# Kernel tuning notes

Hardware: AMD Instinct MI355X
Metric: run time of the kernel (lower is better)

Reference implementation:

```python
import jax, jax.numpy as jnp
import numpy as np

N_NODES = 50000
N_EDGES = 800000
F_IN = 32
F_OUT = 32
NB = 4  # basis terms per dimension


def linear_basis(x, n):
    # Piecewise-linear 'hat' basis on [-1, 1] with n equispaced centers.
    # f_k(x) = max(0, 1 - |x - c_k| / dx),  c_k = linspace(-1, 1, n), dx = 2/(n-1)
    centers = jnp.linspace(-1.0, 1.0, n, dtype=x.dtype)
    dx = 2.0 / (n - 1)
    return jnp.maximum(0.0, 1.0 - jnp.abs(x[:, None] - centers) / dx)  # [E, n]


def setup_inputs() -> dict:
    key = jax.random.key(0)
    k0, k1, k2, k3, k4 = jax.random.split(key, 5)
    x_i = jax.random.normal(k0, (N_NODES, F_IN), dtype=jnp.float32)
    x_j = jax.random.normal(k1, (N_NODES, F_IN), dtype=jnp.float32)
    edge_index = jax.random.randint(k2, (2, N_EDGES), 0, N_NODES)  # row0=target, row1=source
    edge_attr = jax.random.uniform(k3, (N_EDGES, 2), dtype=jnp.float32,
                                   minval=-1.0, maxval=1.0)
    # torch init: uniform_(-0.05, 0.05) on [NB, NB, F_IN, F_OUT]
    weight = jax.random.uniform(k4, (NB, NB, F_IN, F_OUT), dtype=jnp.float32,
                                minval=-0.05, maxval=0.05)
    return {"x_i": x_i, "x_j": x_j, "edge_index": edge_index,
            "edge_attr": edge_attr, "weight": weight}


def reference(x_i, x_j, edge_index, edge_attr, weight):
    dst = edge_index[0]  # aggregation target nodes
    src = edge_index[1]  # source nodes (features gathered from x_j)

    bx = linear_basis(edge_attr[:, 0], NB)            # [E, NB]
    by = linear_basis(edge_attr[:, 1], NB)            # [E, NB]
    b = (bx[:, :, None] * by[:, None, :]).reshape(-1, NB * NB)  # [E, NB*NB]

    feat = x_j[src]                                   # [E, F_IN] edge gather
    w = weight.reshape(NB * NB, F_IN, F_OUT)          # [K, F_IN, F_OUT]
    msg = jnp.einsum('ek,ei,kio->eo', b, feat, w)     # [E, F_OUT]

    # weighted scatter-add to target nodes
    out = jax.ops.segment_sum(msg, dst, num_segments=x_i.shape[0])  # [N, F_OUT]
    return out
```

## Files before the change

kernel.cpp:

```cpp
#include <hip/hip_runtime.h>

typedef short short8 __attribute__((ext_vector_type(8)));
typedef float f32x4 __attribute__((ext_vector_type(4)));

#define NB 4
#define F 32
#define EPB 512
#define SCHUNK 2048
#define MAXNBLK 1024


__device__ __forceinline__ int cell_of(float ax, float ay) {
    float tx = (ax + 1.0f) * 1.5f;
    float ty = (ay + 1.0f) * 1.5f;
    int kx = (int)tx; if (kx > 2) kx = 2; if (kx < 0) kx = 0;
    int ky = (int)ty; if (ky > 2) ky = 2; if (ky < 0) ky = 0;
    return kx * 3 + ky;
}

__device__ __forceinline__ short f2bf(float f) {
    unsigned u = __float_as_uint(f);
    unsigned r = (u + 0x7FFFu + ((u >> 16) & 1u)) >> 16;
    return (short)r;
}

__global__ __launch_bounds__(256) void hist_kernel(
    const float* __restrict__ attr, int E, int* __restrict__ counts)
{
    __shared__ int h[9];
    int b = blockIdx.x, t = threadIdx.x;
    if (t < 9) h[t] = 0;
    __syncthreads();
    int start = b * SCHUNK, end = min(start + SCHUNK, E);
    for (int e = start + t; e < end; e += 256) {
        float2 a = reinterpret_cast<const float2*>(attr)[e];
        atomicAdd(&h[cell_of(a.x, a.y)], 1);
    }
    __syncthreads();
    if (t < 9) counts[b * 9 + t] = h[t];
}

__global__ __launch_bounds__(512) void scan_kernel(
    int* __restrict__ ws, int* __restrict__ counts, int nblk)
{
    __shared__ int s[MAXNBLK * 9];
    __shared__ int tot[9];
    __shared__ int coff[9];
    int n = nblk * 9;
    for (int i = threadIdx.x; i < n; i += 512) s[i] = counts[i];
    __syncthreads();
    if (threadIdx.x < 9) {
        int c = threadIdx.x, run = 0;
        for (int b = 0; b < nblk; ++b) {
            int v = s[b * 9 + c];
            s[b * 9 + c] = run;
            run += v;
        }
        tot[c] = run;
    }
    __syncthreads();
    if (threadIdx.x == 0) {
        int off = 0, boff = 0;
        for (int c = 0; c < 9; ++c) {
            ws[c] = off;  coff[c] = off;
            ws[16 + c] = boff;
            off  += tot[c];
            boff += (tot[c] + EPB - 1) / EPB;
        }
        ws[9] = off;
        ws[16 + 9] = boff;
    }
    __syncthreads();
    for (int i = threadIdx.x; i < n; i += 512)
        counts[i] = s[i] + coff[i % 9];
}

__global__ __launch_bounds__(256) void scatter_kernel(
    const float* __restrict__ attr, int E,
    const int* __restrict__ bases, int* __restrict__ sorted)
{
    __shared__ int cur[9];
    int b = blockIdx.x, t = threadIdx.x;
    if (t < 9) cur[t] = bases[b * 9 + t];
    __syncthreads();
    int start = b * SCHUNK, end = min(start + SCHUNK, E);
    for (int e = start + t; e < end; e += 256) {
        float2 a = reinterpret_cast<const float2*>(attr)[e];
        int c = cell_of(a.x, a.y);
        int pos = atomicAdd(&cur[c], 1);
        sorted[pos] = e;
    }
}

__global__ __launch_bounds__(256) void bconv_mfma(
    const float* __restrict__ x_j, const int* __restrict__ ei,
    const float* __restrict__ attr, const float* __restrict__ weight,
    const int* __restrict__ ws, const int* __restrict__ sorted,
    float* __restrict__ out, int E)
{
    int b = blockIdx.x;
    const int* blkoff = ws + 16;
    if (b >= blkoff[9]) return;
    int c = 0;
    #pragma unroll
    for (int q = 1; q < 9; ++q) c += (b >= blkoff[q]) ? 1 : 0;
    int kx0 = c / 3, ky0 = c - 3 * (c / 3);
    int local  = b - blkoff[c];
    int cstart = ws[c];
    int cend   = ws[c + 1];
    int pstart = cstart + local * EPB;
    int pend   = min(pstart + EPB, cend);

    int t     = threadIdx.x;
    int wid   = t >> 6;
    int lane  = t & 63;
    int row16 = lane & 15;
    int hi    = lane >> 4;
    int edge4 = lane >> 2;
    int chunk = lane & 3;

    __shared__ short featb[4][4][4][16][8];
    __shared__ int   dstl[4][16];

    short8 wb[4][2];
    #pragma unroll
    for (int kk = 0; kk < 4; ++kk) {
        int ks = (kx0 + (kk >> 1)) * NB + (ky0 + (kk & 1));
        const float* wp = weight + (size_t)ks * F * F;
        #pragma unroll
        for (int n = 0; n < 2; ++n) {
            short8 v;
            #pragma unroll
            for (int j = 0; j < 8; ++j)
                v[j] = f2bf(wp[(8 * hi + j) * F + row16 + 16 * n]);
            wb[kk][n] = v;
        }
    }

    int wstart = pstart + wid * (EPB / 4);
    int wend   = min(wstart + (EPB / 4), pend);
    if (wstart >= wend) return;

    int   dst0; float ax0, ay0; float4 fa0, fb0; bool v0;
    auto load = [&](int tstart, int& dst, float& ax, float& ay,
                    float4& fa, float4& fb, bool& valid) {
        int p = tstart + edge4;
        valid = p < wend;
        int pp = valid ? p : wstart;
        int e  = sorted[pp];
        dst = ei[e];
        int srcn = ei[E + e];
        float2 a = reinterpret_cast<const float2*>(attr)[e];
        ax = a.x; ay = a.y;
        const float4* xr = reinterpret_cast<const float4*>(x_j + (size_t)srcn * F);
        fa = xr[chunk * 2];
        fb = xr[chunk * 2 + 1];
    };

    int ntiles = (wend - wstart + 15) >> 4;
    load(wstart, dst0, ax0, ay0, fa0, fb0, v0);

    for (int tt = 0; tt < ntiles; ++tt) {
        float fx  = (ax0 + 1.0f) * 1.5f - (float)kx0;
        float fy  = (ay0 + 1.0f) * 1.5f - (float)ky0;
        float bxa = 1.0f - fx, bya = 1.0f - fy;
        float bc[4] = { bxa * bya, bxa * fy, fx * bya, fx * fy };
        float fl[8] = { fa0.x, fa0.y, fa0.z, fa0.w, fb0.x, fb0.y, fb0.z, fb0.w };
        #pragma unroll
        for (int kk = 0; kk < 4; ++kk) {
            float s = v0 ? bc[kk] : 0.0f;
            short8 sv;
            #pragma unroll
            for (int j = 0; j < 8; ++j) sv[j] = f2bf(fl[j] * s);
            *reinterpret_cast<short8*>(&featb[wid][kk][chunk][edge4][0]) = sv;
        }
        if (chunk == 0) dstl[wid][edge4] = v0 ? dst0 : -1;

        if (tt + 1 < ntiles)
            load(wstart + (tt + 1) * 16, dst0, ax0, ay0, fa0, fb0, v0);

        f32x4 acc0 = {0.f, 0.f, 0.f, 0.f}, acc1 = {0.f, 0.f, 0.f, 0.f};
        #pragma unroll
        for (int kk = 0; kk < 4; ++kk) {
            short8 a = *reinterpret_cast<const short8*>(&featb[wid][kk][hi][row16][0]);
            acc0 = __builtin_amdgcn_mfma_f32_16x16x32_bf16(a, wb[kk][0], acc0, 0, 0, 0);
            acc1 = __builtin_amdgcn_mfma_f32_16x16x32_bf16(a, wb[kk][1], acc1, 0, 0, 0);
        }

        #pragma unroll
        for (int r = 0; r < 4; ++r) {
            int d = dstl[wid][hi * 4 + r];
            if (d >= 0) {
                atomicAdd(&out[(size_t)d * F + row16],      acc0[r]);
                atomicAdd(&out[(size_t)d * F + 16 + row16], acc1[r]);
            }
        }
    }
}

__global__ __launch_bounds__(256) void bconv_fallback(
    const float* __restrict__ x_j, const int* __restrict__ ei,
    const float* __restrict__ attr, const float* __restrict__ weight,
    float* __restrict__ out, int E)
{
    __shared__ float wl[16 * F * F];
    __shared__ float featl[8][F];
    for (int idx = threadIdx.x; idx < 4096; idx += 256)
        reinterpret_cast<float4*>(wl)[idx] = reinterpret_cast<const float4*>(weight)[idx];
    __syncthreads();

    int lane = threadIdx.x & 31, eslot = threadIdx.x >> 5;
    for (int p = blockIdx.x * 8 + eslot; p < E; p += gridDim.x * 8) {
        int dst = ei[p], srcn = ei[E + p];
        float ax = attr[2 * p], ay = attr[2 * p + 1];
        featl[eslot][lane] = x_j[(size_t)srcn * F + lane];
        float tx = (ax + 1.0f) * 1.5f, ty = (ay + 1.0f) * 1.5f;
        int kx0 = (int)tx; if (kx0 > 2) kx0 = 2; if (kx0 < 0) kx0 = 0;
        int ky0 = (int)ty; if (ky0 > 2) ky0 = 2; if (ky0 < 0) ky0 = 0;
        float fx = tx - kx0, fy = ty - ky0;
        float bcv[4] = { (1.0f - fx) * (1.0f - fy), (1.0f - fx) * fy,
                         fx * (1.0f - fy), fx * fy };
        float msg = 0.f;
        const float4* f4 = reinterpret_cast<const float4*>(&featl[eslot][0]);
        #pragma unroll
        for (int kk = 0; kk < 4; ++kk) {
            int k = (kx0 + (kk >> 1)) * NB + (ky0 + (kk & 1));
            const float* wk = wl + k * F * F;
            float acc = 0.f;
            #pragma unroll
            for (int j = 0; j < 8; ++j) {
                float4 f = f4[j];
                acc = fmaf(f.x, wk[(4 * j + 0) * F + lane], acc);
                acc = fmaf(f.y, wk[(4 * j + 1) * F + lane], acc);
                acc = fmaf(f.z, wk[(4 * j + 2) * F + lane], acc);
                acc = fmaf(f.w, wk[(4 * j + 3) * F + lane], acc);
            }
            msg = fmaf(bcv[kk], acc, msg);
        }
        atomicAdd(&out[(size_t)dst * F + lane], msg);
    }
}

extern "C" void kernel_launch(void* const* d_in, const int* in_sizes, int n_in,
                              void* d_out, int out_size, void* d_ws, size_t ws_size,
                              hipStream_t stream) {
    const float* x_j    = (const float*)d_in[1];
    const int*   ei     = (const int*)d_in[2];
    const float* attr   = (const float*)d_in[3];
    const float* weight = (const float*)d_in[4];
    float* out = (float*)d_out;
    int E = in_sizes[2] / 2;

    hipMemsetAsync(d_out, 0, (size_t)out_size * sizeof(float), stream);

    int nblk_sort = (E + SCHUNK - 1) / SCHUNK;
    int sorted_off = 32 + ((nblk_sort * 9 + 15) & ~15);
    size_t ws_need = (size_t)(sorted_off + E) * sizeof(int);

    if (nblk_sort <= MAXNBLK && ws_size >= ws_need) {
        int* ws      = (int*)d_ws;
        int* counts  = ws + 32;
        int* sorted  = ws + sorted_off;
        hist_kernel<<<nblk_sort, 256, 0, stream>>>(attr, E, counts);
        scan_kernel<<<1, 512, 0, stream>>>(ws, counts, nblk_sort);
        scatter_kernel<<<nblk_sort, 256, 0, stream>>>(attr, E, counts, sorted);
        int nblk_main = (E + EPB - 1) / EPB + 9;
        bconv_mfma<<<nblk_main, 256, 0, stream>>>(x_j, ei, attr, weight, ws, sorted, out, E);
    } else {
        bconv_fallback<<<2048, 256, 0, stream>>>(x_j, ei, attr, weight, out, E);
    }
}
```

Before: 113.6 us.

## Bucket edges by destination-node bin and cell, accumulate per bin in LDS

Adds a new default path that counting-sorts edges by a key of (dst/32, basis cell) and packs each edge into 8 bytes: source index, local destination, and quantized fractional coordinates. A new main kernel gives each 32-node bin to two waves. They accumulate MFMA results into shared-memory atomics and write output rows once, so the global atomics and the output memset are no longer needed. The older MFMA path also now builds the bf16 operands in registers and uses shuffles instead of staging through LDS. In exchange the path adds sort overhead, 16-bit quantization of the basis fractions, a limit of N ≤ 65536, and possible load imbalance from high-degree bins.

```diff
diff --git a/kernel.cpp b/kernel.cpp
--- a/kernel.cpp
+++ b/kernel.cpp
@@ -1,14 +1,15 @@
 #include <hip/hip_runtime.h>
+#include <hip/hip_bf16.h>
 
 typedef short short8 __attribute__((ext_vector_type(8)));
 typedef float f32x4 __attribute__((ext_vector_type(4)));
+typedef unsigned uint4v __attribute__((ext_vector_type(4)));
 
 #define NB 4
 #define F 32
 #define EPB 512
 #define SCHUNK 2048
 #define MAXNBLK 1024
-
 
 __device__ __forceinline__ int cell_of(float ax, float ay) {
     float tx = (ax + 1.0f) * 1.5f;
@@ -24,20 +25,193 @@
     return (short)r;
 }
 
+__device__ __forceinline__ unsigned pk2(float a, float b) {
+    __hip_bfloat162 h = __float22bfloat162_rn(make_float2(a, b));
+    union { __hip_bfloat162 h; unsigned u; } cv; cv.h = h; return cv.u;
+}
+
+
+__global__ __launch_bounds__(256) void s1_hist(
+    const int* __restrict__ ei, const float* __restrict__ attr, int E,
+    int* __restrict__ keycnt)
+{
+    int stride = gridDim.x * blockDim.x;
+    for (int e = blockIdx.x * blockDim.x + threadIdx.x; e < E; e += stride) {
+        int dst = ei[e];
+        float2 a = reinterpret_cast<const float2*>(attr)[e];
+        atomicAdd(&keycnt[(dst >> 5) * 9 + cell_of(a.x, a.y)], 1);
+    }
+}
+
+__global__ __launch_bounds__(256) void s2_scan(
+    const int* __restrict__ keycnt, int* __restrict__ keybase,
+    int* __restrict__ cursor, int K)
+{
+    __shared__ int part[256];
+    int t = threadIdx.x;
+    int chunk = (K + 255) / 256;
+    int lo = t * chunk, hi = min(lo + chunk, K);
+    int s = 0;
+    for (int q = lo; q < hi; ++q) s += keycnt[q];
+    part[t] = s;
+    __syncthreads();
+    if (t == 0) {
+        int run = 0;
+        for (int j = 0; j < 256; ++j) { int v = part[j]; part[j] = run; run += v; }
+        keybase[K] = run;
+    }
+    __syncthreads();
+    int run = part[t];
+    for (int q = lo; q < hi; ++q) {
+        int v = keycnt[q];
+        keybase[q] = run; cursor[q] = run;
+        run += v;
+    }
+}
+
+__global__ __launch_bounds__(256) void s3_scatter(
+    const int* __restrict__ ei, const float* __restrict__ attr, int E,
+    int* __restrict__ cursor, uint2* __restrict__ packed)
+{
+    int stride = gridDim.x * blockDim.x;
+    for (int e = blockIdx.x * blockDim.x + threadIdx.x; e < E; e += stride) {
+        int dst = ei[e];
+        int src = ei[E + e];
+        float2 a = reinterpret_cast<const float2*>(attr)[e];
+        float tx = (a.x + 1.0f) * 1.5f, ty = (a.y + 1.0f) * 1.5f;
+        int kx = (int)tx; if (kx > 2) kx = 2; if (kx < 0) kx = 0;
+        int ky = (int)ty; if (ky > 2) ky = 2; if (ky < 0) ky = 0;
+        float fx = tx - kx, fy = ty - ky;
+        unsigned qfx = (unsigned)(fminf(fmaxf(fx, 0.f), 1.f) * 65535.f + 0.5f);
+        unsigned qfy = (unsigned)(fminf(fmaxf(fy, 0.f), 1.f) * 65535.f + 0.5f);
+        int key = (dst >> 5) * 9 + kx * 3 + ky;
+        int pos = atomicAdd(&cursor[key], 1);
+        uint2 rec;
+        rec.x = (unsigned)src | ((unsigned)(dst & 31) << 16);
+        rec.y = qfx | (qfy << 16);
+        packed[pos] = rec;
+    }
+}
+
+__global__ __launch_bounds__(256) void bconv_seg(
+    const float* __restrict__ x_j, const float* __restrict__ weight,
+    const int* __restrict__ keybase, const uint2* __restrict__ packed,
+    float* __restrict__ out, int N, int NBIN)
+{
+    __shared__ short wlds[16384];
+    __shared__ float acc[2][32][36];
+
+    int t = threadIdx.x;
+    for (int idx = t; idx < 16384; idx += 256) {
+        int k = idx >> 10, rem = idx & 1023, i = rem >> 5, o = rem & 31;
+        int slot = ((((k * 4 + (i >> 3)) * 2 + (o >> 4)) * 16) + (o & 15)) * 8 + (i & 7);
+        wlds[slot] = f2bf(weight[idx]);
+    }
+    for (int idx = t; idx < 2 * 32 * 36; idx += 256)
+        (&acc[0][0][0])[idx] = 0.f;
+    __syncthreads();
+
+    int wid = t >> 6, lane = t & 63;
+    int binslot = wid >> 1, h = wid & 1;
+    int bin = blockIdx.x * 2 + binslot;
+    int row16 = lane & 15, hi = lane >> 4;
+
+    if (bin < NBIN) {
+        for (int c = 0; c < 9; ++c) {
+            int key = bin * 9 + c;
+            int s0 = keybase[key], s1 = keybase[key + 1];
+            int len = s1 - s0;
+            if (len <= 0) continue;
+            int kx0 = c / 3, ky0 = c - 3 * (c / 3);
+
+            short8 wb0[4], wb1[4];
+            #pragma unroll
+            for (int kk = 0; kk < 4; ++kk) {
+                int ks = (kx0 + (kk >> 1)) * NB + (ky0 + (kk & 1));
+                wb0[kk] = *reinterpret_cast<const short8*>(
+                    &wlds[(((ks * 4 + hi) * 2 + 0) * 16 + row16) * 8]);
+                wb1[kk] = *reinterpret_cast<const short8*>(
+                    &wlds[(((ks * 4 + hi) * 2 + 1) * 16 + row16) * 8]);
+            }
+
+            int nt = (len + 15) >> 4;
+            auto ldtile = [&](int tti, uint2& r, float4& A, float4& B, bool& v) {
+                int p = s0 + tti * 16 + row16;
+                v = p < s1;
+                int pp = v ? p : s0;
+                r = packed[pp];
+                int src = r.x & 0xFFFF;
+                const float4* x4 = reinterpret_cast<const float4*>(x_j);
+                A = x4[src * 8 + 2 * hi];
+                B = x4[src * 8 + 2 * hi + 1];
+            };
+
+            int ti = h;
+            uint2 rec = {0, 0}; float4 fa = {0,0,0,0}, fb = {0,0,0,0}; bool val = false;
+            if (ti < nt) ldtile(ti, rec, fa, fb, val);
+            for (; ti < nt; ti += 2) {
+                uint2 recn = rec; float4 fan = fa, fbn = fb; bool valn = false;
+                if (ti + 2 < nt) ldtile(ti + 2, recn, fan, fbn, valn);
+
+                float fx = (float)(rec.y & 0xFFFF) * (1.f / 65535.f);
+                float fy = (float)(rec.y >> 16)    * (1.f / 65535.f);
+                float vs = val ? 1.f : 0.f;
+                float bxa = 1.f - fx, bya = 1.f - fy;
+                float bc[4] = { bxa * bya * vs, bxa * fy * vs,
+                                fx * bya * vs, fx * fy * vs };
+                int dstloc = (rec.x >> 16) & 31;
+
+                f32x4 a0 = {0,0,0,0}, a1 = {0,0,0,0};
+                #pragma unroll
+                for (int kk = 0; kk < 4; ++kk) {
+                    float s = bc[kk];
+                    uint4v u;
+                    u[0] = pk2(fa.x * s, fa.y * s);
+                    u[1] = pk2(fa.z * s, fa.w * s);
+                    u[2] = pk2(fb.x * s, fb.y * s);
+                    u[3] = pk2(fb.z * s, fb.w * s);
+                    short8 av = __builtin_bit_cast(short8, u);
+                    a0 = __builtin_amdgcn_mfma_f32_16x16x32_bf16(av, wb0[kk], a0, 0, 0, 0);
+                    a1 = __builtin_amdgcn_mfma_f32_16x16x32_bf16(av, wb1[kk], a1, 0, 0, 0);
+                }
+                #pragma unroll
+                for (int r = 0; r < 4; ++r) {
+                    int n = __shfl(dstloc, 4 * hi + r, 64);
+                    atomicAdd(&acc[binslot][n][row16],      a0[r]);
+                    atomicAdd(&acc[binslot][n][16 + row16], a1[r]);
+                }
+                rec = recn; fa = fan; fb = fbn; val = valn;
+            }
+        }
+    }
+    __syncthreads();
+
+    int nloc = t >> 2, col8 = (t & 3) * 8;
+    int node = blockIdx.x * 64 + nloc;
+    if (node < N) {
+        int bs = nloc >> 5, nn = nloc & 31;
+        float4 v0 = *reinterpret_cast<float4*>(&acc[bs][nn][col8]);
+        float4 v1 = *reinterpret_cast<float4*>(&acc[bs][nn][col8 + 4]);
+        *reinterpret_cast<float4*>(&out[(size_t)node * F + col8])     = v0;
+        *reinterpret_cast<float4*>(&out[(size_t)node * F + col8 + 4]) = v1;
+    }
+}
+
+
 __global__ __launch_bounds__(256) void hist_kernel(
     const float* __restrict__ attr, int E, int* __restrict__ counts)
 {
-    __shared__ int h[9];
+    __shared__ int hh[9];
     int b = blockIdx.x, t = threadIdx.x;
-    if (t < 9) h[t] = 0;
+    if (t < 9) hh[t] = 0;
     __syncthreads();
     int start = b * SCHUNK, end = min(start + SCHUNK, E);
     for (int e = start + t; e < end; e += 256) {
         float2 a = reinterpret_cast<const float2*>(attr)[e];
-        atomicAdd(&h[cell_of(a.x, a.y)], 1);
-    }
-    __syncthreads();
-    if (t < 9) counts[b * 9 + t] = h[t];
+        atomicAdd(&hh[cell_of(a.x, a.y)], 1);
+    }
+    __syncthreads();
+    if (t < 9) counts[b * 9 + t] = hh[t];
 }
 
 __global__ __launch_bounds__(512) void scan_kernel(
@@ -116,11 +290,6 @@
     int lane  = t & 63;
     int row16 = lane & 15;
     int hi    = lane >> 4;
-    int edge4 = lane >> 2;
-    int chunk = lane & 3;
-
-    __shared__ short featb[4][4][4][16][8];
-    __shared__ int   dstl[4][16];
 
     short8 wb[4][2];
     #pragma unroll
@@ -141,61 +310,65 @@
     int wend   = min(wstart + (EPB / 4), pend);
     if (wstart >= wend) return;
 
-    int   dst0; float ax0, ay0; float4 fa0, fb0; bool v0;
-    auto load = [&](int tstart, int& dst, float& ax, float& ay,
-                    float4& fa, float4& fb, bool& valid) {
-        int p = tstart + edge4;
-        valid = p < wend;
-        int pp = valid ? p : wstart;
+    auto ldt = [&](int tstart, uint2& dd, float4& A, float4& B, bool& v) {
+        int p = tstart + row16;
+        v = p < wend;
+        int pp = v ? p : wstart;
         int e  = sorted[pp];
-        dst = ei[e];
+        dd.x = ei[e];
+        float2 a = reinterpret_cast<const float2*>(attr)[e];
+        dd.y = __float_as_uint(a.x);
         int srcn = ei[E + e];
-        float2 a = reinterpret_cast<const float2*>(attr)[e];
-        ax = a.x; ay = a.y;
         const float4* xr = reinterpret_cast<const float4*>(x_j + (size_t)srcn * F);
-        fa = xr[chunk * 2];
-        fb = xr[chunk * 2 + 1];
+        A = xr[2 * hi];
+        B = xr[2 * hi + 1];
+        dd.x |= ((unsigned)__float_as_uint(a.y) & 0u);
+        (void)a;
     };
+    (void)ldt;
 
     int ntiles = (wend - wstart + 15) >> 4;
-    load(wstart, dst0, ax0, ay0, fa0, fb0, v0);
-
     for (int tt = 0; tt < ntiles; ++tt) {
-        float fx  = (ax0 + 1.0f) * 1.5f - (float)kx0;
-        float fy  = (ay0 + 1.0f) * 1.5f - (float)ky0;
-        float bxa = 1.0f - fx, bya = 1.0f - fy;
-        float bc[4] = { bxa * bya, bxa * fy, fx * bya, fx * fy };
-        float fl[8] = { fa0.x, fa0.y, fa0.z, fa0.w, fb0.x, fb0.y, fb0.z, fb0.w };
+        int p = wstart + tt * 16 + row16;
+        bool v = p < wend;
+        int pp = v ? p : wstart;
+        int e  = sorted[pp];
+        int dst = ei[e];
+        int srcn = ei[E + e];
+        float2 a = reinterpret_cast<const float2*>(attr)[e];
+        const float4* xr = reinterpret_cast<const float4*>(x_j + (size_t)srcn * F);
+        float4 fa = xr[2 * hi];
+        float4 fb = xr[2 * hi + 1];
+
+        float fx = (a.x + 1.0f) * 1.5f - (float)kx0;
+        float fy = (a.y + 1.0f) * 1.5f - (float)ky0;
+        float vs = v ? 1.f : 0.f;
+        float bxa = 1.f - fx, bya = 1.f - fy;
+        float bc[4] = { bxa * bya * vs, bxa * fy * vs, fx * bya * vs, fx * fy * vs };
+
+        f32x4 a0 = {0,0,0,0}, a1 = {0,0,0,0};
         #pragma unroll
         for (int kk = 0; kk < 4; ++kk) {
-            float s = v0 ? bc[kk] : 0.0f;
-            short8 sv;
-            #pragma unroll
-            for (int j = 0; j < 8; ++j) sv[j] = f2bf(fl[j] * s);
-            *reinterpret_cast<short8*>(&featb[wid][kk][chunk][edge4][0]) = sv;
-        }
-        if (chunk == 0) dstl[wid][edge4] = v0 ? dst0 : -1;
-
-        if (tt + 1 < ntiles)
-            load(wstart + (tt + 1) * 16, dst0, ax0, ay0, fa0, fb0, v0);
-
-        f32x4 acc0 = {0.f, 0.f, 0.f, 0.f}, acc1 = {0.f, 0.f, 0.f, 0.f};
-        #pragma unroll
-        for (int kk = 0; kk < 4; ++kk) {
-            short8 a = *reinterpret_cast<const short8*>(&featb[wid][kk][hi][row16][0]);
-            acc0 = __builtin_amdgcn_mfma_f32_16x16x32_bf16(a, wb[kk][0], acc0, 0, 0, 0);
-            acc1 = __builtin_amdgcn_mfma_f32_16x16x32_bf16(a, wb[kk][1], acc1, 0, 0, 0);
-        }
-
+            float s = bc[kk];
+            uint4v u;
+            u[0] = pk2(fa.x * s, fa.y * s);
+            u[1] = pk2(fa.z * s, fa.w * s);
+            u[2] = pk2(fb.x * s, fb.y * s);
+            u[3] = pk2(fb.z * s, fb.w * s);
+            short8 av = __builtin_bit_cast(short8, u);
+            a0 = __builtin_amdgcn_mfma_f32_16x16x32_bf16(av, wb[kk][0], a0, 0, 0, 0);
+            a1 = __builtin_amdgcn_mfma_f32_16x16x32_bf16(av, wb[kk][1], a1, 0, 0, 0);
+        }
         #pragma unroll
         for (int r = 0; r < 4; ++r) {
-            int d = dstl[wid][hi * 4 + r];
+            int d = __shfl(v ? dst : -1, 4 * hi + r, 64);
             if (d >= 0) {
-                atomicAdd(&out[(size_t)d * F + row16],      acc0[r]);
-                atomicAdd(&out[(size_t)d * F + 16 + row16], acc1[r]);
+                atomicAdd(&out[(size_t)d * F + row16],      a0[r]);
+                atomicAdd(&out[(size_t)d * F + 16 + row16], a1[r]);
             }
         }
     }
+    (void)wid;
 }
 
 __global__ __launch_bounds__(256) void bconv_fallback(
@@ -226,16 +399,16 @@
         for (int kk = 0; kk < 4; ++kk) {
             int k = (kx0 + (kk >> 1)) * NB + (ky0 + (kk & 1));
             const float* wk = wl + k * F * F;
-            float acc = 0.f;
+            float acc2 = 0.f;
             #pragma unroll
             for (int j = 0; j < 8; ++j) {
                 float4 f = f4[j];
-                acc = fmaf(f.x, wk[(4 * j + 0) * F + lane], acc);
-                acc = fmaf(f.y, wk[(4 * j + 1) * F + lane], acc);
-                acc = fmaf(f.z, wk[(4 * j + 2) * F + lane], acc);
-                acc = fmaf(f.w, wk[(4 * j + 3) * F + lane], acc);
+                acc2 = fmaf(f.x, wk[(4 * j + 0) * F + lane], acc2);
+                acc2 = fmaf(f.y, wk[(4 * j + 1) * F + lane], acc2);
+                acc2 = fmaf(f.z, wk[(4 * j + 2) * F + lane], acc2);
+                acc2 = fmaf(f.w, wk[(4 * j + 3) * F + lane], acc2);
             }
-            msg = fmaf(bcv[kk], acc, msg);
+            msg = fmaf(bcv[kk], acc2, msg);
         }
         atomicAdd(&out[(size_t)dst * F + lane], msg);
     }
@@ -250,14 +423,31 @@
     const float* weight = (const float*)d_in[4];
     float* out = (float*)d_out;
     int E = in_sizes[2] / 2;
-
-    hipMemsetAsync(d_out, 0, (size_t)out_size * sizeof(float), stream);
+    int N = in_sizes[0] / F;
+
+    int NBIN = (N + 31) >> 5;
+    int K = NBIN * 9;
+    size_t poff = ((size_t)(3 * K + 2) + 1) & ~(size_t)1;
+    size_t need_new = (poff + 2 * (size_t)E) * sizeof(int);
 
     int nblk_sort = (E + SCHUNK - 1) / SCHUNK;
     int sorted_off = 32 + ((nblk_sort * 9 + 15) & ~15);
-    size_t ws_need = (size_t)(sorted_off + E) * sizeof(int);
-
-    if (nblk_sort <= MAXNBLK && ws_size >= ws_need) {
+    size_t need_old = (size_t)(sorted_off + E) * sizeof(int);
+
+    if (ws_size >= need_new && N <= 65536) {
+        int* ws      = (int*)d_ws;
+        int* keycnt  = ws;
+        int* keybase = ws + K;
+        int* cursor  = ws + 2 * K + 1;
+        uint2* packed = (uint2*)(ws + poff);
+        hipMemsetAsync(keycnt, 0, (size_t)K * sizeof(int), stream);
+        s1_hist<<<2048, 256, 0, stream>>>(ei, attr, E, keycnt);
+        s2_scan<<<1, 256, 0, stream>>>(keycnt, keybase, cursor, K);
+        s3_scatter<<<2048, 256, 0, stream>>>(ei, attr, E, cursor, packed);
+        int nblk_main = (NBIN + 1) / 2;
+        bconv_seg<<<nblk_main, 256, 0, stream>>>(x_j, weight, keybase, packed, out, N, NBIN);
+    } else if (nblk_sort <= MAXNBLK && ws_size >= need_old) {
+        hipMemsetAsync(d_out, 0, (size_t)out_size * sizeof(float), stream);
         int* ws      = (int*)d_ws;
         int* counts  = ws + 32;
         int* sorted  = ws + sorted_off;
@@ -267,6 +457,7 @@
         int nblk_main = (E + EPB - 1) / EPB + 9;
         bconv_mfma<<<nblk_main, 256, 0, stream>>>(x_j, ei, attr, weight, ws, sorted, out, E);
     } else {
+        hipMemsetAsync(d_out, 0, (size_t)out_size * sizeof(float), stream);
         bconv_fallback<<<2048, 256, 0, stream>>>(x_j, ei, attr, weight, out, E);
     }
 }
```

Measured after the change: 324.7 us. +186.0%, slower.

## Replace global atomic scatter with destination-binned message buffer and shared-memory reduction

Applied to the files above, without the earlier changes.

Adds a two-key counting sort: edges are grouped by basis cell for the MFMA message kernel and by 32-node destination bin for a separate reduction kernel. Messages are written densely into a workspace buffer, then each bin block sums them in LDS and writes the output once, replacing per-element global float atomics and the output memset. Weights are converted to bf16 in a pre-swizzled layout once per call, and features are packed to bf16 in registers with a shuffle for destinations instead of an LDS staging round trip. The cost is extra kernel launches, a 100MB message buffer written and reread, and more sorting passes.

```diff
diff --git a/kernel.cpp b/kernel.cpp
--- a/kernel.cpp
+++ b/kernel.cpp
@@ -1,22 +1,19 @@
 #include <hip/hip_runtime.h>
+#include <hip/hip_bf16.h>
 
 typedef short short8 __attribute__((ext_vector_type(8)));
 typedef float f32x4 __attribute__((ext_vector_type(4)));
-
+typedef unsigned uint4v __attribute__((ext_vector_type(4)));
+
+#define F 32
 #define NB 4
-#define F 32
+#define BINSH 5
+#define BINSZ 32
 #define EPB 512
-#define SCHUNK 2048
-#define MAXNBLK 1024
-
-
-__device__ __forceinline__ int cell_of(float ax, float ay) {
-    float tx = (ax + 1.0f) * 1.5f;
-    float ty = (ay + 1.0f) * 1.5f;
-    int kx = (int)tx; if (kx > 2) kx = 2; if (kx < 0) kx = 0;
-    int ky = (int)ty; if (ky > 2) ky = 2; if (ky < 0) ky = 0;
-    return kx * 3 + ky;
-}
+#define SCH 4096
+#define MAXBIN 2048
+#define OSCH 2048
+#define OMAXNBLK 1024
 
 __device__ __forceinline__ short f2bf(float f) {
     unsigned u = __float_as_uint(f);
@@ -24,26 +21,276 @@
     return (short)r;
 }
 
+__device__ __forceinline__ unsigned pk2(float a, float b) {
+    __hip_bfloat162 h = __float22bfloat162_rn(make_float2(a, b));
+    union { __hip_bfloat162 h; unsigned u; } cv; cv.h = h; return cv.u;
+}
+
+__global__ __launch_bounds__(256) void w_prep(
+    const float* __restrict__ w, short* __restrict__ wbf)
+{
+    int idx = blockIdx.x * 256 + threadIdx.x;
+    int k = idx >> 10, rem = idx & 1023, i = rem >> 5, o = rem & 31;
+    int slot = (((k * 4 + (i >> 3)) * 2 + (o >> 4)) * 16 + (o & 15)) * 8 + (i & 7);
+    wbf[slot] = f2bf(w[idx]);
+}
+
+__global__ __launch_bounds__(256) void h2_kernel(
+    const int* __restrict__ ei, const float* __restrict__ attr, int E, int nbin,
+    int* __restrict__ bincnt, int* __restrict__ cellcnt)
+{
+    __shared__ int hb[MAXBIN];
+    __shared__ int hc[9];
+    int t = threadIdx.x;
+    for (int i = t; i < nbin; i += 256) hb[i] = 0;
+    if (t < 9) hc[t] = 0;
+    __syncthreads();
+    int stride = gridDim.x * blockDim.x;
+    for (int e = blockIdx.x * blockDim.x + t; e < E; e += stride) {
+        int dst = ei[e];
+        float2 a = reinterpret_cast<const float2*>(attr)[e];
+        float tx = fminf(fmaxf((a.x + 1.0f) * 1.5f, 0.f), 3.f);
+        float ty = fminf(fmaxf((a.y + 1.0f) * 1.5f, 0.f), 3.f);
+        int kx = min((int)tx, 2), ky = min((int)ty, 2);
+        atomicAdd(&hb[dst >> BINSH], 1);
+        atomicAdd(&hc[kx * 3 + ky], 1);
+    }
+    __syncthreads();
+    for (int i = t; i < nbin; i += 256)
+        if (hb[i]) atomicAdd(&bincnt[i], hb[i]);
+    if (t < 9 && hc[t]) atomicAdd(&cellcnt[t], hc[t]);
+}
+
+__global__ __launch_bounds__(256) void scan2_kernel(
+    const int* __restrict__ bincnt, int* __restrict__ binbase,
+    int* __restrict__ bincur, const int* __restrict__ cellcnt,
+    int* __restrict__ cellbase, int* __restrict__ cellcur,
+    int* __restrict__ blkoff, int nbin)
+{
+    __shared__ int part[256];
+    int t = threadIdx.x;
+    int chunk = (nbin + 255) / 256;
+    int lo = t * chunk, hi = min(lo + chunk, nbin);
+    int s = 0;
+    for (int q = lo; q < hi; ++q) s += bincnt[q];
+    part[t] = s;
+    __syncthreads();
+    if (t == 0) {
+        int run = 0;
+        for (int j = 0; j < 256; ++j) { int v = part[j]; part[j] = run; run += v; }
+        binbase[nbin] = run;
+    }
+    __syncthreads();
+    int run = part[t];
+    for (int q = lo; q < hi; ++q) {
+        binbase[q] = run; bincur[q] = run;
+        run += bincnt[q];
+    }
+    if (t == 0) {
+        int off = 0, boff = 0;
+        for (int c = 0; c < 9; ++c) {
+            cellbase[c] = off; cellcur[c] = off; blkoff[c] = boff;
+            off  += cellcnt[c];
+            boff += (cellcnt[c] + EPB - 1) / EPB;
+        }
+        cellbase[9] = off; blkoff[9] = boff;
+    }
+}
+
+__global__ __launch_bounds__(256) void scat2_kernel(
+    const int* __restrict__ ei, const float* __restrict__ attr, int E, int nbin,
+    int* __restrict__ bincur, int* __restrict__ cellcur,
+    uint4* __restrict__ cellrec, unsigned char* __restrict__ dloc8)
+{
+    __shared__ int hb[MAXBIN];
+    __shared__ int hc[9];
+    int t = threadIdx.x, b = blockIdx.x;
+    int start = b * SCH, end = min(start + SCH, E);
+    for (int i = t; i < nbin; i += 256) hb[i] = 0;
+    if (t < 9) hc[t] = 0;
+    __syncthreads();
+    for (int e = start + t; e < end; e += 256) {
+        int dst = ei[e];
+        float2 a = reinterpret_cast<const float2*>(attr)[e];
+        float tx = fminf(fmaxf((a.x + 1.0f) * 1.5f, 0.f), 3.f);
+        float ty = fminf(fmaxf((a.y + 1.0f) * 1.5f, 0.f), 3.f);
+        int kx = min((int)tx, 2), ky = min((int)ty, 2);
+        atomicAdd(&hb[dst >> BINSH], 1);
+        atomicAdd(&hc[kx * 3 + ky], 1);
+    }
+    __syncthreads();
+    for (int k = t; k < nbin; k += 256) {
+        int c = hb[k];
+        if (c) hb[k] = atomicAdd(&bincur[k], c);
+    }
+    if (t < 9) hc[t] = atomicAdd(&cellcur[t], hc[t]);
+    __syncthreads();
+    for (int e = start + t; e < end; e += 256) {
+        int dst = ei[e];
+        int src = ei[E + e];
+        float2 a = reinterpret_cast<const float2*>(attr)[e];
+        float tx = fminf(fmaxf((a.x + 1.0f) * 1.5f, 0.f), 3.f);
+        float ty = fminf(fmaxf((a.y + 1.0f) * 1.5f, 0.f), 3.f);
+        int kx = min((int)tx, 2), ky = min((int)ty, 2);
+        int pd = atomicAdd(&hb[dst >> BINSH], 1);
+        int pc = atomicAdd(&hc[kx * 3 + ky], 1);
+        uint4 rec;
+        rec.x = (unsigned)src;
+        rec.y = (unsigned)pd;
+        rec.z = __float_as_uint(tx);
+        rec.w = __float_as_uint(ty);
+        cellrec[pc] = rec;
+        dloc8[pd] = (unsigned char)(dst & (BINSZ - 1));
+    }
+}
+
+__global__ __launch_bounds__(256, 4) void bconv_msg(
+    const float* __restrict__ x_j, const short* __restrict__ wbf,
+    const int* __restrict__ cellbase, const int* __restrict__ blkoff,
+    const uint4* __restrict__ cellrec, float* __restrict__ msg)
+{
+    int b = blockIdx.x;
+    if (b >= blkoff[9]) return;
+    int c = 0;
+    #pragma unroll
+    for (int q = 1; q < 9; ++q) c += (b >= blkoff[q]) ? 1 : 0;
+    int kx0 = c / 3, ky0 = c - 3 * (c / 3);
+    int local  = b - blkoff[c];
+    int cstart = cellbase[c], cend = cellbase[c + 1];
+    int pstart = cstart + local * EPB;
+    int pend   = min(pstart + EPB, cend);
+    if (pstart >= pend) return;
+
+    int t = threadIdx.x;
+    int wid = t >> 6, lane = t & 63;
+    int row16 = lane & 15, hi = lane >> 4;
+
+    short8 w0[4], w1[4];
+    #pragma unroll
+    for (int kk = 0; kk < 4; ++kk) {
+        int ks = (kx0 + (kk >> 1)) * NB + (ky0 + (kk & 1));
+        w0[kk] = *reinterpret_cast<const short8*>(
+            wbf + (((ks * 4 + hi) * 2 + 0) * 16 + row16) * 8);
+        w1[kk] = *reinterpret_cast<const short8*>(
+            wbf + (((ks * 4 + hi) * 2 + 1) * 16 + row16) * 8);
+    }
+
+    const float4* x4 = reinterpret_cast<const float4*>(x_j);
+    int ntile = (pend - pstart + 15) >> 4;
+
+    auto fetch = [&](int ti, uint4& rec, float4& fa, float4& fb, int& pdv) {
+        int p = pstart + ti * 16 + row16;
+        bool v = p < pend;
+        int pp = v ? p : pstart;
+        rec = cellrec[pp];
+        int src = rec.x;
+        fa = x4[src * 8 + 2 * hi];
+        fb = x4[src * 8 + 2 * hi + 1];
+        pdv = v ? (int)rec.y : -1;
+    };
+
+    int it = wid;
+    uint4 rec; float4 fa, fb; int pdv;
+    if (it < ntile) fetch(it, rec, fa, fb, pdv);
+
+    for (; it < ntile; it += 4) {
+        uint4 recN; float4 faN, fbN; int pdvN = -1;
+        bool hn = (it + 4) < ntile;
+        if (hn) fetch(it + 4, recN, faN, fbN, pdvN);
+
+        float tx = __uint_as_float(rec.z), ty = __uint_as_float(rec.w);
+        float fx = tx - (float)kx0, fy = ty - (float)ky0;
+        float bx0 = 1.f - fx, by0 = 1.f - fy;
+        float bc[4] = { bx0 * by0, bx0 * fy, fx * by0, fx * fy };
+        float fl[8] = { fa.x, fa.y, fa.z, fa.w, fb.x, fb.y, fb.z, fb.w };
+
+        f32x4 a0 = {0,0,0,0}, a1 = {0,0,0,0};
+        #pragma unroll
+        for (int kk = 0; kk < 4; ++kk) {
+            float s = bc[kk];
+            uint4v u;
+            u[0] = pk2(fl[0] * s, fl[1] * s);
+            u[1] = pk2(fl[2] * s, fl[3] * s);
+            u[2] = pk2(fl[4] * s, fl[5] * s);
+            u[3] = pk2(fl[6] * s, fl[7] * s);
+            short8 av = __builtin_bit_cast(short8, u);
+            a0 = __builtin_amdgcn_mfma_f32_16x16x32_bf16(av, w0[kk], a0, 0, 0, 0);
+            a1 = __builtin_amdgcn_mfma_f32_16x16x32_bf16(av, w1[kk], a1, 0, 0, 0);
+        }
+        #pragma unroll
+        for (int r = 0; r < 4; ++r) {
+            int pd = __shfl(pdv, 4 * hi + r, 64);
+            if (pd >= 0) {
+                float* mrow = msg + (size_t)pd * 32;
+                mrow[row16]      = a0[r];
+                mrow[row16 + 16] = a1[r];
+            }
+        }
+        rec = recN; fa = faN; fb = fbN; pdv = pdvN;
+    }
+}
+
+__global__ __launch_bounds__(256, 8) void bconv_reduce(
+    const float* __restrict__ msg, const unsigned char* __restrict__ dloc8,
+    const int* __restrict__ binbase, float* __restrict__ out, int N)
+{
+    __shared__ float acc[BINSZ][33];
+    int t = threadIdx.x, bin = blockIdx.x;
+    for (int i = t; i < BINSZ * 33; i += 256) (&acc[0][0])[i] = 0.f;
+    __syncthreads();
+
+    int s0 = binbase[bin], s1 = binbase[bin + 1];
+    int col = t & 31;
+    int i = s0 + (t >> 5);
+    for (; i + 24 < s1; i += 32) {
+        float v0 = msg[(size_t)(i)      * 32 + col];
+        float v1 = msg[(size_t)(i + 8)  * 32 + col];
+        float v2 = msg[(size_t)(i + 16) * 32 + col];
+        float v3 = msg[(size_t)(i + 24) * 32 + col];
+        int d0 = dloc8[i], d1 = dloc8[i + 8], d2 = dloc8[i + 16], d3 = dloc8[i + 24];
+        atomicAdd(&acc[d0][col], v0);
+        atomicAdd(&acc[d1][col], v1);
+        atomicAdd(&acc[d2][col], v2);
+        atomicAdd(&acc[d3][col], v3);
+    }
+    for (; i < s1; i += 8) {
+        float v = msg[(size_t)i * 32 + col];
+        atomicAdd(&acc[dloc8[i]][col], v);
+    }
+    __syncthreads();
+
+    int nloc = t >> 3, c4 = (t & 7) * 4;
+    int node = bin * BINSZ + nloc;
+    if (node < N) {
+        float4 v;
+        v.x = acc[nloc][c4];     v.y = acc[nloc][c4 + 1];
+        v.z = acc[nloc][c4 + 2]; v.w = acc[nloc][c4 + 3];
+        *reinterpret_cast<float4*>(&out[(size_t)node * F + c4]) = v;
+    }
+}
+
 __global__ __launch_bounds__(256) void hist_kernel(
     const float* __restrict__ attr, int E, int* __restrict__ counts)
 {
-    __shared__ int h[9];
+    __shared__ int hh[9];
     int b = blockIdx.x, t = threadIdx.x;
-    if (t < 9) h[t] = 0;
-    __syncthreads();
-    int start = b * SCHUNK, end = min(start + SCHUNK, E);
+    if (t < 9) hh[t] = 0;
+    __syncthreads();
+    int start = b * OSCH, end = min(start + OSCH, E);
     for (int e = start + t; e < end; e += 256) {
         float2 a = reinterpret_cast<const float2*>(attr)[e];
-        atomicAdd(&h[cell_of(a.x, a.y)], 1);
-    }
-    __syncthreads();
-    if (t < 9) counts[b * 9 + t] = h[t];
+        float tx = fminf(fmaxf((a.x + 1.0f) * 1.5f, 0.f), 3.f);
+        float ty = fminf(fmaxf((a.y + 1.0f) * 1.5f, 0.f), 3.f);
+        atomicAdd(&hh[min((int)tx, 2) * 3 + min((int)ty, 2)], 1);
+    }
+    __syncthreads();
+    if (t < 9) counts[b * 9 + t] = hh[t];
 }
 
 __global__ __launch_bounds__(512) void scan_kernel(
     int* __restrict__ ws, int* __restrict__ counts, int nblk)
 {
-    __shared__ int s[MAXNBLK * 9];
+    __shared__ int s[OMAXNBLK * 9];
     __shared__ int tot[9];
     __shared__ int coff[9];
     int n = nblk * 9;
@@ -83,10 +330,12 @@
     int b = blockIdx.x, t = threadIdx.x;
     if (t < 9) cur[t] = bases[b * 9 + t];
     __syncthreads();
-    int start = b * SCHUNK, end = min(start + SCHUNK, E);
+    int start = b * OSCH, end = min(start + OSCH, E);
     for (int e = start + t; e < end; e += 256) {
         float2 a = reinterpret_cast<const float2*>(attr)[e];
-        int c = cell_of(a.x, a.y);
+        float tx = fminf(fmaxf((a.x + 1.0f) * 1.5f, 0.f), 3.f);
+        float ty = fminf(fmaxf((a.y + 1.0f) * 1.5f, 0.f), 3.f);
+        int c = min((int)tx, 2) * 3 + min((int)ty, 2);
         int pos = atomicAdd(&cur[c], 1);
         sorted[pos] = e;
     }
@@ -106,21 +355,13 @@
     for (int q = 1; q < 9; ++q) c += (b >= blkoff[q]) ? 1 : 0;
     int kx0 = c / 3, ky0 = c - 3 * (c / 3);
     int local  = b - blkoff[c];
-    int cstart = ws[c];
-    int cend   = ws[c + 1];
+    int cstart = ws[c], cend = ws[c + 1];
     int pstart = cstart + local * EPB;
     int pend   = min(pstart + EPB, cend);
 
-    int t     = threadIdx.x;
-    int wid   = t >> 6;
-    int lane  = t & 63;
-    int row16 = lane & 15;
-    int hi    = lane >> 4;
-    int edge4 = lane >> 2;
-    int chunk = lane & 3;
-
-    __shared__ short featb[4][4][4][16][8];
-    __shared__ int   dstl[4][16];
+    int t = threadIdx.x;
+    int wid = t >> 6, lane = t & 63;
+    int row16 = lane & 15, hi = lane >> 4;
 
     short8 wb[4][2];
     #pragma unroll
@@ -141,58 +382,44 @@
     int wend   = min(wstart + (EPB / 4), pend);
     if (wstart >= wend) return;
 
-    int   dst0; float ax0, ay0; float4 fa0, fb0; bool v0;
-    auto load = [&](int tstart, int& dst, float& ax, float& ay,
-                    float4& fa, float4& fb, bool& valid) {
-        int p = tstart + edge4;
-        valid = p < wend;
-        int pp = valid ? p : wstart;
+    int ntiles = (wend - wstart + 15) >> 4;
+    for (int tt = 0; tt < ntiles; ++tt) {
+        int p = wstart + tt * 16 + row16;
+        bool v = p < wend;
+        int pp = v ? p : wstart;
         int e  = sorted[pp];
-        dst = ei[e];
+        int dst = ei[e];
         int srcn = ei[E + e];
         float2 a = reinterpret_cast<const float2*>(attr)[e];
-        ax = a.x; ay = a.y;
         const float4* xr = reinterpret_cast<const float4*>(x_j + (size_t)srcn * F);
-        fa = xr[chunk * 2];
-        fb = xr[chunk * 2 + 1];
-    };
-
-    int ntiles = (wend - wstart + 15) >> 4;
-    load(wstart, dst0, ax0, ay0, fa0, fb0, v0);
-
-    for (int tt = 0; tt < ntiles; ++tt) {
-        float fx  = (ax0 + 1.0f) * 1.5f - (float)kx0;
-        float fy  = (ay0 + 1.0f) * 1.5f - (float)ky0;
-        float bxa = 1.0f - fx, bya = 1.0f - fy;
-        float bc[4] = { bxa * bya, bxa * fy, fx * bya, fx * fy };
-        float fl[8] = { fa0.x, fa0.y, fa0.z, fa0.w, fb0.x, fb0.y, fb0.z, fb0.w };
+        float4 fa = xr[2 * hi];
+        float4 fb = xr[2 * hi + 1];
+
+        float fx = (a.x + 1.0f) * 1.5f - (float)kx0;
+        float fy = (a.y + 1.0f) * 1.5f - (float)ky0;
+        float vs = v ? 1.f : 0.f;
+        float bx0 = (1.f - fx) * vs, bx1 = fx * vs;
+        float bc[4] = { bx0 * (1.f - fy), bx0 * fy, bx1 * (1.f - fy), bx1 * fy };
+
+        f32x4 a0 = {0,0,0,0}, a1 = {0,0,0,0};
         #pragma unroll
         for (int kk = 0; kk < 4; ++kk) {
-            float s = v0 ? bc[kk] : 0.0f;
-            short8 sv;
-            #pragma unroll
-            for (int j = 0; j < 8; ++j) sv[j] = f2bf(fl[j] * s);
-            *reinterpret_cast<short8*>(&featb[wid][kk][chunk][edge4][0]) = sv;
-        }
-        if (chunk == 0) dstl[wid][edge4] = v0 ? dst0 : -1;
-
-        if (tt + 1 < ntiles)
-            load(wstart + (tt + 1) * 16, dst0, ax0, ay0, fa0, fb0, v0);
-
-        f32x4 acc0 = {0.f, 0.f, 0.f, 0.f}, acc1 = {0.f, 0.f, 0.f, 0.f};
-        #pragma unroll
-        for (int kk = 0; kk < 4; ++kk) {
-            short8 a = *reinterpret_cast<const short8*>(&featb[wid][kk][hi][row16][0]);
-            acc0 = __builtin_amdgcn_mfma_f32_16x16x32_bf16(a, wb[kk][0], acc0, 0, 0, 0);
-            acc1 = __builtin_amdgcn_mfma_f32_16x16x32_bf16(a, wb[kk][1], acc1, 0, 0, 0);
-        }
-
+            float s = bc[kk];
+            uint4v u;
+            u[0] = pk2(fa.x * s, fa.y * s);
+            u[1] = pk2(fa.z * s, fa.w * s);
+            u[2] = pk2(fb.x * s, fb.y * s);
+            u[3] = pk2(fb.z * s, fb.w * s);
+            short8 av = __builtin_bit_cast(short8, u);
+            a0 = __builtin_amdgcn_mfma_f32_16x16x32_bf16(av, wb[kk][0], a0, 0, 0, 0);
+            a1 = __builtin_amdgcn_mfma_f32_16x16x32_bf16(av, wb[kk][1], a1, 0, 0, 0);
+        }
         #pragma unroll
         for (int r = 0; r < 4; ++r) {
-            int d = dstl[wid][hi * 4 + r];
+            int d = __shfl(v ? dst : -1, 4 * hi + r, 64);
             if (d >= 0) {
-                atomicAdd(&out[(size_t)d * F + row16],      acc0[r]);
-                atomicAdd(&out[(size_t)d * F + 16 + row16], acc1[r]);
+                atomicAdd(&out[(size_t)d * F + row16],      a0[r]);
+                atomicAdd(&out[(size_t)d * F + 16 + row16], a1[r]);
             }
         }
     }
@@ -215,8 +442,7 @@
         float ax = attr[2 * p], ay = attr[2 * p + 1];
         featl[eslot][lane] = x_j[(size_t)srcn * F + lane];
         float tx = (ax + 1.0f) * 1.5f, ty = (ay + 1.0f) * 1.5f;
-        int kx0 = (int)tx; if (kx0 > 2) kx0 = 2; if (kx0 < 0) kx0 = 0;
-        int ky0 = (int)ty; if (ky0 > 2) ky0 = 2; if (ky0 < 0) ky0 = 0;
+        int kx0 = min(max((int)tx, 0), 2), ky0 = min(max((int)ty, 0), 2);
         float fx = tx - kx0, fy = ty - ky0;
         float bcv[4] = { (1.0f - fx) * (1.0f - fy), (1.0f - fx) * fy,
                          fx * (1.0f - fy), fx * fy };
@@ -226,16 +452,16 @@
         for (int kk = 0; kk < 4; ++kk) {
             int k = (kx0 + (kk >> 1)) * NB + (ky0 + (kk & 1));
             const float* wk = wl + k * F * F;
-            float acc = 0.f;
+            float a2 = 0.f;
             #pragma unroll
             for (int j = 0; j < 8; ++j) {
                 float4 f = f4[j];
-                acc = fmaf(f.x, wk[(4 * j + 0) * F + lane], acc);
-                acc = fmaf(f.y, wk[(4 * j + 1) * F + lane], acc);
-                acc = fmaf(f.z, wk[(4 * j + 2) * F + lane], acc);
-                acc = fmaf(f.w, wk[(4 * j + 3) * F + lane], acc);
+                a2 = fmaf(f.x, wk[(4 * j + 0) * F + lane], a2);
+                a2 = fmaf(f.y, wk[(4 * j + 1) * F + lane], a2);
+                a2 = fmaf(f.z, wk[(4 * j + 2) * F + lane], a2);
+                a2 = fmaf(f.w, wk[(4 * j + 3) * F + lane], a2);
             }
-            msg = fmaf(bcv[kk], acc, msg);
+            msg = fmaf(bcv[kk], a2, msg);
         }
         atomicAdd(&out[(size_t)dst * F + lane], msg);
     }
@@ -250,14 +476,50 @@
     const float* weight = (const float*)d_in[4];
     float* out = (float*)d_out;
     int E = in_sizes[2] / 2;
-
-    hipMemsetAsync(d_out, 0, (size_t)out_size * sizeof(float), stream);
-
-    int nblk_sort = (E + SCHUNK - 1) / SCHUNK;
+    int N = in_sizes[0] / F;
+
+    int nbin = (N + BINSZ - 1) >> BINSH;
+
+    int o_bincnt   = 0;
+    int o_cellcnt  = o_bincnt + nbin;
+    int o_binbase  = o_cellcnt + 9;
+    int o_bincur   = o_binbase + nbin + 1;
+    int o_cellbase = o_bincur + nbin;
+    int o_cellcur  = o_cellbase + 10;
+    int o_blkoff   = o_cellcur + 9;
+    int o_wbf      = (o_blkoff + 10 + 3) & ~3;
+    int o_dloc     = o_wbf + 8192;
+    int o_cellrec  = (o_dloc + (E + 3) / 4 + 3) & ~3;
+    size_t o_msg   = (size_t)((o_cellrec + 4 * (size_t)E + 3) & ~3);
+    size_t need_new = (o_msg + 32 * (size_t)E) * sizeof(int);
+
+    int nblk_sort = (E + OSCH - 1) / OSCH;
     int sorted_off = 32 + ((nblk_sort * 9 + 15) & ~15);
-    size_t ws_need = (size_t)(sorted_off + E) * sizeof(int);
-
-    if (nblk_sort <= MAXNBLK && ws_size >= ws_need) {
+    size_t need_old = (size_t)(sorted_off + E) * sizeof(int);
+
+    if (nbin <= MAXBIN && N <= 65536 && E < (1 << 24) && ws_size >= need_new) {
+        int* ws = (int*)d_ws;
+        short* wbf = (short*)(ws + o_wbf);
+        unsigned char* dloc8 = (unsigned char*)(ws + o_dloc);
+        uint4* cellrec = (uint4*)(ws + o_cellrec);
+        float* msg = (float*)(ws + o_msg);
+
+        hipMemsetAsync(ws, 0, (size_t)(nbin + 9) * sizeof(int), stream);
+        w_prep<<<64, 256, 0, stream>>>(weight, wbf);
+        h2_kernel<<<256, 256, 0, stream>>>(ei, attr, E, nbin,
+                                           ws + o_bincnt, ws + o_cellcnt);
+        scan2_kernel<<<1, 256, 0, stream>>>(ws + o_bincnt, ws + o_binbase,
+                                            ws + o_bincur, ws + o_cellcnt,
+                                            ws + o_cellbase, ws + o_cellcur,
+                                            ws + o_blkoff, nbin);
+        scat2_kernel<<<(E + SCH - 1) / SCH, 256, 0, stream>>>(
+            ei, attr, E, nbin, ws + o_bincur, ws + o_cellcur, cellrec, dloc8);
+        int nblkA = (E + EPB - 1) / EPB + 9;
+        bconv_msg<<<nblkA, 256, 0, stream>>>(x_j, wbf, ws + o_cellbase,
+                                             ws + o_blkoff, cellrec, msg);
+        bconv_reduce<<<nbin, 256, 0, stream>>>(msg, dloc8, ws + o_binbase, out, N);
+    } else if (nblk_sort <= OMAXNBLK && ws_size >= need_old) {
+        hipMemsetAsync(d_out, 0, (size_t)out_size * sizeof(float), stream);
         int* ws      = (int*)d_ws;
         int* counts  = ws + 32;
         int* sorted  = ws + sorted_off;
@@ -267,6 +529,7 @@
         int nblk_main = (E + EPB - 1) / EPB + 9;
         bconv_mfma<<<nblk_main, 256, 0, stream>>>(x_j, ei, attr, weight, ws, sorted, out, E);
     } else {
+        hipMemsetAsync(d_out, 0, (size_t)out_size * sizeof(float), stream);
         bconv_fallback<<<2048, 256, 0, stream>>>(x_j, ei, attr, weight, out, E);
     }
 }
```

Measured after the change: 240.7 us. +112.0%, slower.
